# Kernel tuning notes

Hardware: AMD Instinct MI355X
Metric: run time of the kernel (lower is better)

Reference implementation:

```python
import jax, jax.numpy as jnp
import numpy as np

BN_EPS = 1e-5


def conv3x3(x, w):
    # 3x3 'same' conv, stride 1, no bias (matches nn.Conv2d(k=3, padding=1, bias=False))
    return jax.lax.conv_general_dilated(
        x, w, window_strides=(1, 1), padding='SAME',
        dimension_numbers=('NCHW', 'OIHW', 'NCHW'))


def batchnorm(x, gamma, beta, mean, var):
    # eval-mode BatchNorm2d with running stats
    scale = (gamma / jnp.sqrt(var + BN_EPS))[None, :, None, None]
    return (x - mean[None, :, None, None]) * scale + beta[None, :, None, None]


def setup_inputs() -> dict:
    key = jax.random.key(0)
    ks = jax.random.split(key, 13)
    B, C, H, W = 16, 64, 160, 160
    wshape = (C, C, 3, 3)
    inp = {
        'x': jax.random.normal(ks[0], (B, C, H, W), jnp.float32),
        'w_cv1': jax.random.normal(ks[1], wshape, jnp.float32) * 0.05,
        'g1': jax.random.uniform(ks[2], (C,), jnp.float32, 0.5, 1.5),
        'b1': jax.random.normal(ks[3], (C,), jnp.float32) * 0.1,
        'm1': jax.random.normal(ks[4], (C,), jnp.float32) * 0.1,
        'v1': jax.random.uniform(ks[5], (C,), jnp.float32, 0.5, 1.5),
        'wq': jax.random.normal(ks[6], wshape, jnp.float32) * 0.05,
        'wk': jax.random.normal(ks[7], wshape, jnp.float32) * 0.05,
        'wv': jax.random.normal(ks[8], wshape, jnp.float32) * 0.05,
        'g2': jax.random.uniform(ks[9], (C,), jnp.float32, 0.5, 1.5),
        'b2': jax.random.normal(ks[10], (C,), jnp.float32) * 0.1,
        'm2': jax.random.normal(ks[11], (C,), jnp.float32) * 0.1,
        'v2': jax.random.uniform(ks[12], (C,), jnp.float32, 0.5, 1.5),
    }
    return inp


def reference(x, w_cv1, g1, b1, m1, v1, wq, wk, wv, g2, b2, m2, v2):
    # cv1: Conv -> BN -> SiLU
    y = jax.nn.silu(batchnorm(conv3x3(x, w_cv1), g1, b1, m1, v1))

    # CSA_ConvBlock on y (c_ channels)
    fq = conv3x3(y, wq)   # [B,C,H,W]
    fk = conv3x3(y, wk)
    fv = conv3x3(y, wv)
    H, W = y.shape[2], y.shape[3]

    # Original: f_sim[b,i,j,h1,h2] = sum_w fq[b,i,h1,w]*fk[b,j,h2,w] / sqrt(W);
    # then sum over j, then mean-ish sum over (h1,h2)/H^2 -> f_scores[b,i].
    # Algebraically identical reorder (sum-before-matmul):
    k_sum = fk.sum(axis=(1, 2))                       # [B,W], sum over channels j and rows h2
    scale = 1.0 / (float(W) ** 0.5 * float(H) * float(H))
    f_scores = jnp.einsum('bchw,bw->bc', fq, k_sum) * scale  # [B,C]
    scores = jax.nn.softmax(f_scores, axis=1)[:, :, None, None]

    r = scores * fv + y
    r = jax.nn.relu(batchnorm(r, g2, b2, m2, v2))

    # shortcut: c1 == c2 and shortcut=True
    return x + r
```

## Files before the change

kernel.cpp:

```cpp
#include <hip/hip_runtime.h>
#include <hip/hip_bf16.h>
#include <math.h>

#define NB 16
#define NC 64
#define NH 160
#define NW 160

typedef __attribute__((ext_vector_type(8))) short bf16x8;
typedef __attribute__((ext_vector_type(4))) float f32x4;
typedef __attribute__((ext_vector_type(8))) unsigned short u16x8;
typedef __attribute__((ext_vector_type(4))) unsigned short u16x4;

__device__ __forceinline__ unsigned short f2bf(float v) {
  union { __hip_bfloat16 b; unsigned short u; } cv; cv.b = __float2bfloat16(v); return cv.u;
}
__device__ __forceinline__ float bf2f(unsigned short u) {
  union { unsigned u; float f; } cv; cv.u = ((unsigned)u) << 16; return cv.f;
}

#define LGKM_BARRIER()                                  \
  asm volatile("s_waitcnt lgkmcnt(0)" ::: "memory");    \
  __builtin_amdgcn_sched_barrier(0);                    \
  __builtin_amdgcn_s_barrier();                         \
  __builtin_amdgcn_sched_barrier(0);

__global__ void pack_w_kernel3(const float* __restrict__ wA, const float* __restrict__ wB,
                               const float* __restrict__ wq, const float* __restrict__ wk,
                               unsigned short* __restrict__ apkA, unsigned short* __restrict__ apkB,
                               float* __restrict__ wqt, float* __restrict__ wkst) {
  int idx = blockIdx.x * 256 + threadIdx.x;
  if (idx < 2 * 36864) {
    const float* w = (idx < 36864) ? wA : wB;
    unsigned short* apk = (idx < 36864) ? apkA : apkB;
    int i = (idx < 36864) ? idx : idx - 36864;
    int j = i & 7, l = (i >> 3) & 63, rest = i >> 9;
    int ks = rest % 18, ct = rest / 18;
    int cih = ks & 1, tap = ks >> 1, kh = tap / 3, kw = tap % 3;
    int co = ct * 16 + (l & 15), ci = cih * 32 + (l >> 4) * 8 + j;
    apk[i] = f2bf(w[(((size_t)co * NC + ci) * 3 + kh) * 3 + kw]);
  } else if (idx < 3 * 36864) {
    int i2 = idx - 2 * 36864;
    int c = i2 & 63, tau = i2 >> 6;
    int i = tau & 63, jj = tau >> 6;
    wqt[i2] = wq[(size_t)c * 576 + i * 9 + jj];
  } else if (idx < 3 * 36864 + 576) {
    int i3 = idx - 3 * 36864;
    int i = i3 & 63, jj = i3 >> 6;
    float s = 0.f;
    for (int cj = 0; cj < NC; ++cj) s += wk[(size_t)cj * 576 + i * 9 + jj];
    wkst[i3] = s;
  }
}

template<bool FINAL>
__global__ __launch_bounds__(256, 2) void conv3x3_mfma7(
    const unsigned short* __restrict__ in_nhwc, const float* __restrict__ in_nchw,
    const unsigned short* __restrict__ apk,
    const float* __restrict__ gg, const float* __restrict__ bbeta,
    const float* __restrict__ mmean, const float* __restrict__ vvar,
    void* __restrict__ outv, const float* __restrict__ scores,
    const float* __restrict__ xres, float* __restrict__ colpart)
{
  __shared__ unsigned short ring[6 * 34 * 64];
  __shared__ unsigned short epi[FINAL ? 8 : 2 * 64 * 72];
  __shared__ f32x4 csv[FINAL ? 1 : 512];

  const int t = threadIdx.x, lane = t & 63, wave = t >> 6;
  const int q = lane >> 4, col = lane & 15;

  int g = blockIdx.x;
  int sw = (g & 7) * 160 + (g >> 3);
  const int b = sw / 80;
  int rem = sw % 80;
  const int h0 = (rem / 5) * 10, w0 = (rem % 5) * 32;

  float scR[4], shR[4], scoR[4];
#pragma unroll
  for (int r = 0; r < 4; ++r) {
    int co = wave * 16 + q * 4 + r;
    float s = gg[co] * rsqrtf(vvar[co] + 1e-5f);
    scR[r] = s; shR[r] = bbeta[co] - mmean[co] * s;
    scoR[r] = FINAL ? scores[b * NC + co] : 0.f;
  }

  bf16x8 wf[18];
#pragma unroll
  for (int ks = 0; ks < 18; ++ks)
    wf[ks] = *(const bf16x8*)&apk[((size_t)(wave * 18 + ks) * 64 + lane) * 8];

  const unsigned short* inb = FINAL ? in_nhwc + (size_t)b * NH * NW * 64 : nullptr;
  const float* xb = FINAL ? nullptr : in_nchw + (size_t)b * NC * NH * NW;

#define SLOT(R) ((int)((unsigned)((R) + 1) % 6u) * 2176)

#define STGF_ISSUE(ROW, V0, V1, A0, A1)                                       \
  { int row_ = (ROW);                                                         \
    bool rowok_ = (unsigned)row_ < (unsigned)NH;                              \
    int slot_ = SLOT(row_);                                                   \
    { int wcc = t >> 3, s8 = t & 7; int wsrc = w0 + wcc - 1;                  \
      A0 = slot_ + wcc * 64 + ((s8 ^ (wcc & 7)) << 3);                        \
      V0 = (u16x8){};                                                         \
      if (rowok_ && (unsigned)wsrc < (unsigned)NW)                            \
        V0 = *(const u16x8*)&inb[((size_t)row_ * NW + wsrc) * 64 + s8 * 8];   \
    }                                                                         \
    if (t < 16) { int c = 256 + t; int wcc = c >> 3, s8 = c & 7;              \
      int wsrc = w0 + wcc - 1;                                                \
      A1 = slot_ + wcc * 64 + ((s8 ^ (wcc & 7)) << 3);                        \
      V1 = (u16x8){};                                                         \
      if (rowok_ && (unsigned)wsrc < (unsigned)NW)                            \
        V1 = *(const u16x8*)&inb[((size_t)row_ * NW + wsrc) * 64 + s8 * 8];   \
    } }
#define STGF_COMMIT(V0, V1, A0, A1)                                           \
  *(u16x8*)&ring[A0] = V0;                                                    \
  if (t < 16) *(u16x8*)&ring[A1] = V1;

#define STG1_ISSUE(ROW, F0, F1, A0, A1)                                       \
  { int row_ = (ROW);                                                         \
    bool rowok_ = (unsigned)row_ < (unsigned)NH;                              \
    int slot_ = SLOT(row_);                                                   \
    { int wcc = t % 34, s8 = t / 34; int wsrc = w0 + wcc - 1;                 \
      A0 = slot_ + wcc * 64 + ((s8 ^ (wcc & 7)) << 3);                        \
      bool ok_ = rowok_ && (unsigned)wsrc < (unsigned)NW;                     \
      if (ok_) {                                                              \
        const float* xp_ = xb + ((size_t)(s8 * 8) * NH + row_) * NW + wsrc;   \
        _Pragma("unroll") for (int j_ = 0; j_ < 8; ++j_)                      \
          F0[j_] = xp_[(size_t)j_ * NH * NW];                                 \
      } else {                                                                \
        _Pragma("unroll") for (int j_ = 0; j_ < 8; ++j_) F0[j_] = 0.f;        \
      }                                                                       \
    }                                                                         \
    if (t < 16) { int wcc = 18 + t; int wsrc = w0 + wcc - 1;                  \
      A1 = slot_ + wcc * 64 + ((7 ^ (wcc & 7)) << 3);                         \
      bool ok_ = rowok_ && (unsigned)wsrc < (unsigned)NW;                     \
      if (ok_) {                                                              \
        const float* xp_ = xb + ((size_t)56 * NH + row_) * NW + wsrc;         \
        _Pragma("unroll") for (int j_ = 0; j_ < 8; ++j_)                      \
          F1[j_] = xp_[(size_t)j_ * NH * NW];                                 \
      } else {                                                                \
        _Pragma("unroll") for (int j_ = 0; j_ < 8; ++j_) F1[j_] = 0.f;        \
      }                                                                       \
    } }
#define STG1_COMMIT(F0, F1, A0, A1)                                           \
  { u16x8 pv_;                                                                \
    _Pragma("unroll") for (int j_ = 0; j_ < 8; ++j_) pv_[j_] = f2bf(F0[j_]);  \
    *(u16x8*)&ring[A0] = pv_; }                                               \
  if (t < 16) { u16x8 pv_;                                                    \
    _Pragma("unroll") for (int j_ = 0; j_ < 8; ++j_) pv_[j_] = f2bf(F1[j_]);  \
    *(u16x8*)&ring[A1] = pv_; }

  if constexpr (!FINAL) {
    csv[t] = (f32x4){0.f, 0.f, 0.f, 0.f};
    csv[t + 256] = (f32x4){0.f, 0.f, 0.f, 0.f};
  }

  if constexpr (FINAL) {
    for (int rr = -1; rr <= 2; ++rr) {
      u16x8 v0, v1 = {}; int a0, a1 = 0;
      STGF_ISSUE(h0 + rr, v0, v1, a0, a1)
      STGF_COMMIT(v0, v1, a0, a1)
    }
  } else {
    for (int rr = -1; rr <= 2; ++rr) {
      float f0[8], f1[8]; int a0, a1 = 0;
      STG1_ISSUE(h0 + rr, f0, f1, a0, a1)
      STG1_COMMIT(f0, f1, a0, a1)
    }
  }
  LGKM_BARRIER()

  for (int wi = 0; wi < 5; ++wi) {
    const int h = h0 + wi * 2;
    const bool doS = (wi < 4);

    u16x8 va0, va1 = {}, vb0, vb1 = {}; int aa0, aa1 = 0, ab0, ab1 = 0;
    float fa0[8], fa1[8], fb0[8], fb1[8];
    if (doS) {
      if constexpr (FINAL) {
        STGF_ISSUE(h + 3, va0, va1, aa0, aa1)
        STGF_ISSUE(h + 4, vb0, vb1, ab0, ab1)
      } else {
        STG1_ISSUE(h + 3, fa0, fa1, aa0, aa1)
        STG1_ISSUE(h + 4, fb0, fb1, ab0, ab1)
      }
    }

    const int sl[4] = { SLOT(h - 1), SLOT(h), SLOT(h + 1), SLOT(h + 2) };
    f32x4 acc[2][2];
#pragma unroll
    for (int o = 0; o < 2; ++o) { acc[o][0] = (f32x4){0,0,0,0}; acc[o][1] = (f32x4){0,0,0,0}; }

#pragma unroll
    for (int ri = 0; ri < 4; ++ri) {
#pragma unroll
      for (int kw = 0; kw < 3; ++kw) {
#pragma unroll
        for (int cih = 0; cih < 2; ++cih) {
          const int wcb = col + kw;
          const int ea = sl[ri] + wcb * 64 + (((cih << 2) + q) ^ (wcb & 7)) * 8;
          const bf16x8* bp = (const bf16x8*)&ring[ea];
          bf16x8 B0 = bp[0], B1 = bp[128];
          if (ri <= 2) {
            const int ks = (ri * 3 + kw) * 2 + cih;
            acc[0][0] = __builtin_amdgcn_mfma_f32_16x16x32_bf16(wf[ks], B0, acc[0][0], 0, 0, 0);
            acc[0][1] = __builtin_amdgcn_mfma_f32_16x16x32_bf16(wf[ks], B1, acc[0][1], 0, 0, 0);
          }
          if (ri >= 1) {
            const int ks = ((ri - 1) * 3 + kw) * 2 + cih;
            acc[1][0] = __builtin_amdgcn_mfma_f32_16x16x32_bf16(wf[ks], B0, acc[1][0], 0, 0, 0);
            acc[1][1] = __builtin_amdgcn_mfma_f32_16x16x32_bf16(wf[ks], B1, acc[1][1], 0, 0, 0);
          }
        }
      }
    }

    if constexpr (!FINAL) {
      const int buf = (wi & 1) * 4608;
      f32x4 csadd[2];
      csadd[0] = (f32x4){0,0,0,0}; csadd[1] = (f32x4){0,0,0,0};
#pragma unroll
      for (int o = 0; o < 2; ++o) {
#pragma unroll
        for (int wt = 0; wt < 2; ++wt) {
          u16x4 ev;
#pragma unroll
          for (int r = 0; r < 4; ++r) {
            float z = scR[r] * acc[o][wt][r] + shR[r];
            ev[r] = f2bf(z / (1.f + __expf(-z)));
          }
          *(u16x4*)&epi[buf + ((o * 32) + wt * 16 + col) * 72 + wave * 16 + q * 4] = ev;
#pragma unroll
          for (int r = 0; r < 4; ++r) csadd[wt][r] += bf2f(ev[r]);
        }
      }
      { int cc = wave * 4 + q;
        csv[cc * 32 + col]      += csadd[0];
        csv[cc * 32 + 16 + col] += csadd[1]; }
      if (doS) { STG1_COMMIT(fa0, fa1, aa0, aa1) STG1_COMMIT(fb0, fb1, ab0, ab1) }
      LGKM_BARRIER()
      { int w = t >> 3, s = t & 7;
#pragma unroll
        for (int o = 0; o < 2; ++o) {
          unsigned short* yo = (unsigned short*)outv + (((size_t)b * NH + h + o) * NW + w0) * 64;
          *(u16x8*)&yo[w * 64 + s * 8] = *(const u16x8*)&epi[buf + ((o * 32) + w) * 72 + s * 8];
        }
      }
    } else {
      if (doS) { STGF_COMMIT(va0, va1, aa0, aa1) STGF_COMMIT(vb0, vb1, ab0, ab1) }
      float* outp = (float*)outv;
#pragma unroll
      for (int o = 0; o < 2; ++o) {
        const int rb1 = sl[1 + o];
#pragma unroll
        for (int wt = 0; wt < 2; ++wt) {
          int wcc = wt * 16 + col + 1;
          int gr = (wave * 2 + (q >> 1)) ^ (wcc & 7);
          u16x4 yv = *(const u16x4*)&ring[rb1 + wcc * 64 + gr * 8 + (q & 1) * 4];
#pragma unroll
          for (int r = 0; r < 4; ++r) {
            int co = wave * 16 + q * 4 + r;
            float rv = scoR[r] * acc[o][wt][r] + bf2f(yv[r]);
            float rb_ = scR[r] * rv + shR[r];
            rb_ = fmaxf(rb_, 0.f);
            size_t oi = (((size_t)b * NC + co) * NH + h + o) * NW + w0 + wt * 16 + col;
            outp[oi] = xres[oi] + rb_;
          }
        }
      }
      LGKM_BARRIER()
    }
  }

  if constexpr (!FINAL) {
    const int strip = h0 / 10;
    float* pp = colpart + (((size_t)b * 16 + strip) * NW + w0) * 64;
    int w = t >> 3, g0 = t & 7;
    *(f32x4*)&pp[w * 64 + g0 * 4]       = csv[g0 * 32 + w];
    *(f32x4*)&pp[w * 64 + (g0 + 8) * 4] = csv[(g0 + 8) * 32 + w];
  }
#undef STG1_ISSUE
#undef STG1_COMMIT
#undef STGF_ISSUE
#undef STGF_COMMIT
#undef SLOT
}

__global__ void colsum2_kernel(const float* __restrict__ part, float* __restrict__ ycol) {
  int id = blockIdx.x * 256 + threadIdx.x;
  if (id >= NB * NW * NC) return;
  int c = id & 63; int bw = id >> 6; int w = bw % NW; int b = bw / NW;
  const float* p = part + (((size_t)b * 16) * NW + w) * 64 + c;
  float s = 0.f;
#pragma unroll
  for (int st = 0; st < 16; ++st) s += p[(size_t)st * NW * 64];
  ycol[id] = s;
}

__device__ __forceinline__ float zval(const float* __restrict__ ycol,
                                      const unsigned short* __restrict__ y,
                                      int b, int i, int kh, int wp) {
  float z = ycol[((size_t)b * NW + wp) * 64 + i];
  if (kh == 0) z -= bf2f(y[(((size_t)b * NH + (NH - 1)) * NW + wp) * 64 + i]);
  if (kh == 2) z -= bf2f(y[(((size_t)b * NH) * NW + wp) * 64 + i]);
  return z;
}

__global__ __launch_bounds__(256) void ks_kernel(
    const float* __restrict__ ycol, const unsigned short* __restrict__ y,
    const float* __restrict__ wkst, float* __restrict__ ks)
{
  int id = blockIdx.x * 4 + (threadIdx.x >> 6);
  int lane = threadIdx.x & 63;
  int b = id / NW, w = id % NW;
  float s = 0.f;
#pragma unroll
  for (int jj = 0; jj < 9; ++jj) {
    int kh = jj / 3, kw = jj % 3;
    int wp = w + kw - 1;
    if ((unsigned)wp < (unsigned)NW)
      s += wkst[jj * 64 + lane] * zval(ycol, y, b, lane, kh, wp);
  }
#pragma unroll
  for (int off = 32; off; off >>= 1) s += __shfl_xor(s, off);
  if (lane == 0) ks[id] = s;
}

__global__ __launch_bounds__(256) void u_kernel(
    const float* __restrict__ ycol, const unsigned short* __restrict__ y,
    const float* __restrict__ ks, float* __restrict__ U)
{
  __shared__ float red[4][64];
  int bid = blockIdx.x;
  int b = bid / 9, jj = bid % 9;
  int kh = jj / 3, kw = jj % 3;
  int i = threadIdx.x & 63, ch = threadIdx.x >> 6;
  float s = 0.f;
  for (int w = ch * 40; w < ch * 40 + 40; ++w) {
    int wp = w + kw - 1;
    if ((unsigned)wp < (unsigned)NW)
      s += zval(ycol, y, b, i, kh, wp) * ks[b * NW + w];
  }
  red[ch][i] = s;
  __syncthreads();
  if (threadIdx.x < 64)
    U[((size_t)b * 9 + jj) * 64 + threadIdx.x] =
        red[0][threadIdx.x] + red[1][threadIdx.x] + red[2][threadIdx.x] + red[3][threadIdx.x];
}

__global__ __launch_bounds__(256) void scores_kernel2(
    const float* __restrict__ wqt, const float* __restrict__ U,
    float* __restrict__ scores)
{
  __shared__ float red[4][64];
  int b = blockIdx.x;
  int c = threadIdx.x & 63, p = threadIdx.x >> 6;
  const float* Ub = U + (size_t)b * 576;
  float s = 0.f;
  for (int tau = p * 144; tau < p * 144 + 144; ++tau)
    s += wqt[(size_t)tau * 64 + c] * Ub[tau];
  red[p][c] = s;
  __syncthreads();
  if (threadIdx.x < 64) {
    const float scale = 1.0f / (sqrtf((float)NW) * (float)NH * (float)NH);
    float f = (red[0][c] + red[1][c] + red[2][c] + red[3][c]) * scale;
    float mx = f;
#pragma unroll
    for (int off = 32; off; off >>= 1) mx = fmaxf(mx, __shfl_xor(mx, off));
    float e = __expf(f - mx);
    float sm = e;
#pragma unroll
    for (int off = 32; off; off >>= 1) sm += __shfl_xor(sm, off);
    scores[b * NC + c] = e / sm;
  }
}

extern "C" void kernel_launch(void* const* d_in, const int* in_sizes, int n_in,
                              void* d_out, int out_size, void* d_ws, size_t ws_size,
                              hipStream_t stream) {
  const float* x  = (const float*)d_in[0];
  const float* w1 = (const float*)d_in[1];
  const float* g1 = (const float*)d_in[2];
  const float* b1 = (const float*)d_in[3];
  const float* m1 = (const float*)d_in[4];
  const float* v1 = (const float*)d_in[5];
  const float* wq = (const float*)d_in[6];
  const float* wk = (const float*)d_in[7];
  const float* wv = (const float*)d_in[8];
  const float* g2 = (const float*)d_in[9];
  const float* b2 = (const float*)d_in[10];
  const float* m2 = (const float*)d_in[11];
  const float* v2 = (const float*)d_in[12];
  float* out = (float*)d_out;

  unsigned short* apk1 = (unsigned short*)d_ws;
  unsigned short* apk2 = apk1 + 36864;
  float* wqt  = (float*)(apk2 + 36864);
  float* wkst = wqt + 36864;
  float* ycol = wkst + 576;
  float* ks   = ycol + NB * NW * NC;
  float* U    = ks + NB * NW;
  float* scr  = U + NB * 576;
  float* part = scr + 1024;
  unsigned short* y = (unsigned short*)(part + (size_t)NB * 16 * NW * 64);

  pack_w_kernel3<<<dim3(435), 256, 0, stream>>>(w1, wv, wq, wk, apk1, apk2, wqt, wkst);

  conv3x3_mfma7<false><<<dim3(1280), 256, 0, stream>>>(
      nullptr, x, apk1, g1, b1, m1, v1, (void*)y, nullptr, nullptr, part);

  colsum2_kernel<<<dim3((NB * NW * NC + 255) / 256), 256, 0, stream>>>(part, ycol);
  ks_kernel<<<dim3(NB * NW / 4), 256, 0, stream>>>(ycol, y, wkst, ks);
  u_kernel<<<dim3(NB * 9), 256, 0, stream>>>(ycol, y, ks, U);
  scores_kernel2<<<dim3(NB), 256, 0, stream>>>(wqt, U, scr);

  conv3x3_mfma7<true><<<dim3(1280), 256, 0, stream>>>(
      y, nullptr, apk2, g2, b2, m2, v2, (void*)out, scr, x, nullptr);
}
```

Baseline: 150.4 us.

## Deepen row prefetch pipeline, preload residual, and raise MFMA wave priority

Row staging changes from a one-step in-iteration load to a two-row-ahead software pipeline. Global loads for rows h+5/h+6 are issued before the MFMA loop and committed to the LDS ring at the start of the next iteration, and the prologue overlaps pairs of row loads. The final pass also loads the residual x values before the MFMA loop instead of in the epilogue, and s_setprio raises wave priority around the MFMA block. The aim is to hide global memory latency behind compute, at the cost of more live registers, which could cause spills at 2 blocks per CU. Correctness depends on the ring slots not being overwritten while still being read.

```diff
diff --git a/kernel.cpp b/kernel.cpp
--- a/kernel.cpp
+++ b/kernel.cpp
@@ -54,7 +54,7 @@
 }
 
 template<bool FINAL>
-__global__ __launch_bounds__(256, 2) void conv3x3_mfma7(
+__global__ __launch_bounds__(256, 2) void conv3x3_mfma8(
     const unsigned short* __restrict__ in_nhwc, const float* __restrict__ in_nchw,
     const unsigned short* __restrict__ apk,
     const float* __restrict__ gg, const float* __restrict__ bbeta,
@@ -154,35 +154,67 @@
     csv[t + 256] = (f32x4){0.f, 0.f, 0.f, 0.f};
   }
 
+  u16x8 pva0, pva1 = {}, pvb0, pvb1 = {};
+  float pfa0[8], pfa1[8], pfb0[8], pfb1[8];
+  int paa0, paa1 = 0, pab0, pab1 = 0;
+
   if constexpr (FINAL) {
-    for (int rr = -1; rr <= 2; ++rr) {
-      u16x8 v0, v1 = {}; int a0, a1 = 0;
-      STGF_ISSUE(h0 + rr, v0, v1, a0, a1)
-      STGF_COMMIT(v0, v1, a0, a1)
-    }
+    { u16x8 v0, v1 = {}, w0v, w1v = {}; int a0, a1 = 0, b0a, b1a = 0;
+      STGF_ISSUE(h0 - 1, v0, v1, a0, a1)
+      STGF_ISSUE(h0,     w0v, w1v, b0a, b1a)
+      STGF_COMMIT(v0, v1, a0, a1) STGF_COMMIT(w0v, w1v, b0a, b1a)
+      STGF_ISSUE(h0 + 1, v0, v1, a0, a1)
+      STGF_ISSUE(h0 + 2, w0v, w1v, b0a, b1a)
+      STGF_COMMIT(v0, v1, a0, a1) STGF_COMMIT(w0v, w1v, b0a, b1a) }
+    STGF_ISSUE(h0 + 3, pva0, pva1, paa0, paa1)
+    STGF_ISSUE(h0 + 4, pvb0, pvb1, pab0, pab1)
   } else {
-    for (int rr = -1; rr <= 2; ++rr) {
-      float f0[8], f1[8]; int a0, a1 = 0;
-      STG1_ISSUE(h0 + rr, f0, f1, a0, a1)
-      STG1_COMMIT(f0, f1, a0, a1)
-    }
+    { float f0[8], f1[8], g0[8], g1[8]; int a0, a1 = 0, b0a, b1a = 0;
+      STG1_ISSUE(h0 - 1, f0, f1, a0, a1)
+      STG1_ISSUE(h0,     g0, g1, b0a, b1a)
+      STG1_COMMIT(f0, f1, a0, a1) STG1_COMMIT(g0, g1, b0a, b1a)
+      STG1_ISSUE(h0 + 1, f0, f1, a0, a1)
+      STG1_ISSUE(h0 + 2, g0, g1, b0a, b1a)
+      STG1_COMMIT(f0, f1, a0, a1) STG1_COMMIT(g0, g1, b0a, b1a) }
+    STG1_ISSUE(h0 + 3, pfa0, pfa1, paa0, paa1)
+    STG1_ISSUE(h0 + 4, pfb0, pfb1, pab0, pab1)
   }
   LGKM_BARRIER()
 
+#pragma unroll
   for (int wi = 0; wi < 5; ++wi) {
     const int h = h0 + wi * 2;
-    const bool doS = (wi < 4);
-
-    u16x8 va0, va1 = {}, vb0, vb1 = {}; int aa0, aa1 = 0, ab0, ab1 = 0;
-    float fa0[8], fa1[8], fb0[8], fb1[8];
-    if (doS) {
+
+    if (wi < 4) {
       if constexpr (FINAL) {
-        STGF_ISSUE(h + 3, va0, va1, aa0, aa1)
-        STGF_ISSUE(h + 4, vb0, vb1, ab0, ab1)
+        STGF_COMMIT(pva0, pva1, paa0, paa1)
+        STGF_COMMIT(pvb0, pvb1, pab0, pab1)
       } else {
-        STG1_ISSUE(h + 3, fa0, fa1, aa0, aa1)
-        STG1_ISSUE(h + 4, fb0, fb1, ab0, ab1)
-      }
+        STG1_COMMIT(pfa0, pfa1, paa0, paa1)
+        STG1_COMMIT(pfb0, pfb1, pab0, pab1)
+      }
+    }
+    if (wi < 3) {
+      if constexpr (FINAL) {
+        STGF_ISSUE(h + 5, pva0, pva1, paa0, paa1)
+        STGF_ISSUE(h + 6, pvb0, pvb1, pab0, pab1)
+      } else {
+        STG1_ISSUE(h + 5, pfa0, pfa1, paa0, paa1)
+        STG1_ISSUE(h + 6, pfb0, pfb1, pab0, pab1)
+      }
+    }
+
+    float xrv[2][2][4];
+    if constexpr (FINAL) {
+#pragma unroll
+      for (int o = 0; o < 2; ++o)
+#pragma unroll
+        for (int wt = 0; wt < 2; ++wt)
+#pragma unroll
+          for (int r = 0; r < 4; ++r) {
+            int co = wave * 16 + q * 4 + r;
+            xrv[o][wt][r] = xres[(((size_t)b * NC + co) * NH + h + o) * NW + w0 + wt * 16 + col];
+          }
     }
 
     const int sl[4] = { SLOT(h - 1), SLOT(h), SLOT(h + 1), SLOT(h + 2) };
@@ -190,6 +222,7 @@
 #pragma unroll
     for (int o = 0; o < 2; ++o) { acc[o][0] = (f32x4){0,0,0,0}; acc[o][1] = (f32x4){0,0,0,0}; }
 
+    __builtin_amdgcn_s_setprio(1);
 #pragma unroll
     for (int ri = 0; ri < 4; ++ri) {
 #pragma unroll
@@ -213,6 +246,7 @@
         }
       }
     }
+    __builtin_amdgcn_s_setprio(0);
 
     if constexpr (!FINAL) {
       const int buf = (wi & 1) * 4608;
@@ -236,7 +270,6 @@
       { int cc = wave * 4 + q;
         csv[cc * 32 + col]      += csadd[0];
         csv[cc * 32 + 16 + col] += csadd[1]; }
-      if (doS) { STG1_COMMIT(fa0, fa1, aa0, aa1) STG1_COMMIT(fb0, fb1, ab0, ab1) }
       LGKM_BARRIER()
       { int w = t >> 3, s = t & 7;
 #pragma unroll
@@ -246,7 +279,6 @@
         }
       }
     } else {
-      if (doS) { STGF_COMMIT(va0, va1, aa0, aa1) STGF_COMMIT(vb0, vb1, ab0, ab1) }
       float* outp = (float*)outv;
 #pragma unroll
       for (int o = 0; o < 2; ++o) {
@@ -263,7 +295,7 @@
             float rb_ = scR[r] * rv + shR[r];
             rb_ = fmaxf(rb_, 0.f);
             size_t oi = (((size_t)b * NC + co) * NH + h + o) * NW + w0 + wt * 16 + col;
-            outp[oi] = xres[oi] + rb_;
+            outp[oi] = xrv[o][wt][r] + rb_;
           }
         }
       }
@@ -405,7 +437,7 @@
 
   pack_w_kernel3<<<dim3(435), 256, 0, stream>>>(w1, wv, wq, wk, apk1, apk2, wqt, wkst);
 
-  conv3x3_mfma7<false><<<dim3(1280), 256, 0, stream>>>(
+  conv3x3_mfma8<false><<<dim3(1280), 256, 0, stream>>>(
       nullptr, x, apk1, g1, b1, m1, v1, (void*)y, nullptr, nullptr, part);
 
   colsum2_kernel<<<dim3((NB * NW * NC + 255) / 256), 256, 0, stream>>>(part, ycol);
@@ -413,6 +445,6 @@
   u_kernel<<<dim3(NB * 9), 256, 0, stream>>>(ycol, y, ks, U);
   scores_kernel2<<<dim3(NB), 256, 0, stream>>>(wqt, U, scr);
 
-  conv3x3_mfma7<true><<<dim3(1280), 256, 0, stream>>>(
+  conv3x3_mfma8<true><<<dim3(1280), 256, 0, stream>>>(
       y, nullptr, apk2, g2, b2, m2, v2, (void*)out, scr, x, nullptr);
 }
```

Measured after the change: 162.5 us. 8.1% more time.

## Compute three output rows per window with deeper ring and register column sums

Applied to the files above, without the earlier changes.

The conv kernel now splits each 10-row strip into 3+3+2+2 output rows instead of five 2-row windows, with a fully unrolled schedule and an 8-slot input ring. Each staged input row then feeds more MFMAs per barrier, and there are fewer barriers and window iterations. Column sums stay in registers and are written once through the reused epilogue buffer, which removes the per-window LDS read-modify-write. In exchange the kernel holds more accumulators and needs more LDS, which may cut occupancy at the launch bound of 2 blocks per CU.

```diff
diff --git a/kernel.cpp b/kernel.cpp
--- a/kernel.cpp
+++ b/kernel.cpp
@@ -54,7 +54,7 @@
 }
 
 template<bool FINAL>
-__global__ __launch_bounds__(256, 2) void conv3x3_mfma7(
+__global__ __launch_bounds__(256, 2) void conv3x3_mfma10(
     const unsigned short* __restrict__ in_nhwc, const float* __restrict__ in_nchw,
     const unsigned short* __restrict__ apk,
     const float* __restrict__ gg, const float* __restrict__ bbeta,
@@ -62,9 +62,8 @@
     void* __restrict__ outv, const float* __restrict__ scores,
     const float* __restrict__ xres, float* __restrict__ colpart)
 {
-  __shared__ unsigned short ring[6 * 34 * 64];
-  __shared__ unsigned short epi[FINAL ? 8 : 2 * 64 * 72];
-  __shared__ f32x4 csv[FINAL ? 1 : 512];
+  __shared__ unsigned short ring[8 * 34 * 64];
+  __shared__ unsigned short epi[FINAL ? 8 : 2 * 3 * 32 * 72];
 
   const int t = threadIdx.x, lane = t & 63, wave = t >> 6;
   const int q = lane >> 4, col = lane & 15;
@@ -89,10 +88,14 @@
   for (int ks = 0; ks < 18; ++ks)
     wf[ks] = *(const bf16x8*)&apk[((size_t)(wave * 18 + ks) * 64 + lane) * 8];
 
+  f32x4 csreg[2];
+  csreg[0] = (f32x4){0.f, 0.f, 0.f, 0.f};
+  csreg[1] = (f32x4){0.f, 0.f, 0.f, 0.f};
+
   const unsigned short* inb = FINAL ? in_nhwc + (size_t)b * NH * NW * 64 : nullptr;
   const float* xb = FINAL ? nullptr : in_nchw + (size_t)b * NC * NH * NW;
 
-#define SLOT(R) ((int)((unsigned)((R) + 1) % 6u) * 2176)
+#define SLOT(R) ((int)((unsigned)((R) + 1) % 8u) * 2176)
 
 #define STGF_ISSUE(ROW, V0, V1, A0, A1)                                       \
   { int row_ = (ROW);                                                         \
@@ -149,139 +152,171 @@
     _Pragma("unroll") for (int j_ = 0; j_ < 8; ++j_) pv_[j_] = f2bf(F1[j_]);  \
     *(u16x8*)&ring[A1] = pv_; }
 
+#define COMPUTE_RI(NR, RI)                                                    \
+  { const int slr = SLOT(h - 1 + (RI));                                       \
+    _Pragma("unroll") for (int kw = 0; kw < 3; ++kw) {                        \
+      _Pragma("unroll") for (int cih = 0; cih < 2; ++cih) {                   \
+        const int wcb = col + kw;                                             \
+        const int ea = slr + wcb * 64 + (((cih << 2) + q) ^ (wcb & 7)) * 8;   \
+        const bf16x8* bp = (const bf16x8*)&ring[ea];                          \
+        bf16x8 B0 = bp[0], B1 = bp[128];                                      \
+        _Pragma("unroll") for (int o = 0; o < (NR); ++o) {                    \
+          if (o <= (RI) && (RI) - o <= 2) {                                   \
+            const int ksx = (((RI) - o) * 3 + kw) * 2 + cih;                  \
+            acc[o][0] = __builtin_amdgcn_mfma_f32_16x16x32_bf16(wf[ksx], B0, acc[o][0], 0, 0, 0); \
+            acc[o][1] = __builtin_amdgcn_mfma_f32_16x16x32_bf16(wf[ksx], B1, acc[o][1], 0, 0, 0); \
+          } } } } }
+
+#define EPILOGUE(NR, WI)                                                      \
+    if constexpr (!FINAL) {                                                   \
+      const int buf = ((WI) & 1) * 6912;                                      \
+      _Pragma("unroll") for (int o = 0; o < (NR); ++o) {                      \
+        _Pragma("unroll") for (int wt = 0; wt < 2; ++wt) {                    \
+          u16x4 ev;                                                           \
+          _Pragma("unroll") for (int r = 0; r < 4; ++r) {                     \
+            float z = scR[r] * acc[o][wt][r] + shR[r];                        \
+            ev[r] = f2bf(z / (1.f + __expf(-z)));                             \
+          }                                                                   \
+          *(u16x4*)&epi[buf + ((o * 32) + wt * 16 + col) * 72 + wave * 16 + q * 4] = ev; \
+          _Pragma("unroll") for (int r = 0; r < 4; ++r)                       \
+            csreg[wt][r] += bf2f(ev[r]);                                      \
+        } }                                                                   \
+      LGKM_BARRIER()                                                          \
+      { int w_ = t >> 3, s_ = t & 7;                                          \
+        _Pragma("unroll") for (int o = 0; o < (NR); ++o) {                    \
+          unsigned short* yo = (unsigned short*)outv +                        \
+              (((size_t)b * NH + h + o) * NW + w0) * 64;                      \
+          *(u16x8*)&yo[w_ * 64 + s_ * 8] =                                    \
+              *(const u16x8*)&epi[buf + ((o * 32) + w_) * 72 + s_ * 8];       \
+        } }                                                                   \
+    } else {                                                                  \
+      float* outp = (float*)outv;                                             \
+      _Pragma("unroll") for (int o = 0; o < (NR); ++o) {                      \
+        const int rb1 = SLOT(h + o);                                          \
+        _Pragma("unroll") for (int wt = 0; wt < 2; ++wt) {                    \
+          int wcc = wt * 16 + col + 1;                                        \
+          int gr = (wave * 2 + (q >> 1)) ^ (wcc & 7);                         \
+          u16x4 yv = *(const u16x4*)&ring[rb1 + wcc * 64 + gr * 8 + (q & 1) * 4]; \
+          _Pragma("unroll") for (int r = 0; r < 4; ++r) {                     \
+            int co = wave * 16 + q * 4 + r;                                   \
+            float rv = scoR[r] * acc[o][wt][r] + bf2f(yv[r]);                 \
+            float rb_ = scR[r] * rv + shR[r];                                 \
+            rb_ = fmaxf(rb_, 0.f);                                            \
+            size_t oi = (((size_t)b * NC + co) * NH + h + o) * NW + w0 + wt * 16 + col; \
+            outp[oi] = xres[oi] + rb_;                                        \
+          } } }                                                               \
+      LGKM_BARRIER()                                                          \
+    }
+
+#define DO_WIN3(WI, HOFF, SN)                                                 \
+  { const int h = h0 + (HOFF);                                                \
+    u16x8 v10, v11 = {}, v20, v21 = {};                                       \
+    float f10[8], f11[8], f20[8], f21[8];                                     \
+    int a10 = 0, a11 = 0, a20 = 0, a21 = 0;                                   \
+    if constexpr (FINAL) {                                                    \
+      if ((SN) >= 1) STGF_ISSUE(h + 4, v10, v11, a10, a11)                    \
+      if ((SN) >= 2) STGF_ISSUE(h + 5, v20, v21, a20, a21)                    \
+    } else {                                                                  \
+      if ((SN) >= 1) STG1_ISSUE(h + 4, f10, f11, a10, a11)                    \
+      if ((SN) >= 2) STG1_ISSUE(h + 5, f20, f21, a20, a21)                    \
+    }                                                                         \
+    f32x4 acc[3][2];                                                          \
+    _Pragma("unroll") for (int o = 0; o < 3; ++o) {                           \
+      acc[o][0] = (f32x4){0.f,0.f,0.f,0.f}; acc[o][1] = (f32x4){0.f,0.f,0.f,0.f}; } \
+    COMPUTE_RI(3, 0) COMPUTE_RI(3, 1)                                         \
+    if constexpr (FINAL) {                                                    \
+      if ((SN) >= 1) { STGF_COMMIT(v10, v11, a10, a11) }                      \
+      if ((SN) >= 2) { STGF_COMMIT(v20, v21, a20, a21) }                      \
+      if ((SN) >= 3) STGF_ISSUE(h + 6, v10, v11, a10, a11)                    \
+    } else {                                                                  \
+      if ((SN) >= 1) { STG1_COMMIT(f10, f11, a10, a11) }                      \
+      if ((SN) >= 2) { STG1_COMMIT(f20, f21, a20, a21) }                      \
+      if ((SN) >= 3) STG1_ISSUE(h + 6, f10, f11, a10, a11)                    \
+    }                                                                         \
+    COMPUTE_RI(3, 2) COMPUTE_RI(3, 3) COMPUTE_RI(3, 4)                        \
+    if constexpr (FINAL) {                                                    \
+      if ((SN) >= 3) { STGF_COMMIT(v10, v11, a10, a11) }                      \
+    } else {                                                                  \
+      if ((SN) >= 3) { STG1_COMMIT(f10, f11, a10, a11) }                      \
+    }                                                                         \
+    EPILOGUE(3, WI)                                                           \
+  }
+
+#define DO_WIN2(WI, HOFF, SN)                                                 \
+  { const int h = h0 + (HOFF);                                                \
+    u16x8 v10, v11 = {}, v20, v21 = {};                                       \
+    float f10[8], f11[8], f20[8], f21[8];                                     \
+    int a10 = 0, a11 = 0, a20 = 0, a21 = 0;                                   \
+    if constexpr (FINAL) {                                                    \
+      if ((SN) >= 1) STGF_ISSUE(h + 3, v10, v11, a10, a11)                    \
+      if ((SN) >= 2) STGF_ISSUE(h + 4, v20, v21, a20, a21)                    \
+    } else {                                                                  \
+      if ((SN) >= 1) STG1_ISSUE(h + 3, f10, f11, a10, a11)                    \
+      if ((SN) >= 2) STG1_ISSUE(h + 4, f20, f21, a20, a21)                    \
+    }                                                                         \
+    f32x4 acc[2][2];                                                          \
+    _Pragma("unroll") for (int o = 0; o < 2; ++o) {                           \
+      acc[o][0] = (f32x4){0.f,0.f,0.f,0.f}; acc[o][1] = (f32x4){0.f,0.f,0.f,0.f}; } \
+    COMPUTE_RI(2, 0) COMPUTE_RI(2, 1)                                         \
+    if constexpr (FINAL) {                                                    \
+      if ((SN) >= 1) { STGF_COMMIT(v10, v11, a10, a11) }                      \
+      if ((SN) >= 2) { STGF_COMMIT(v20, v21, a20, a21) }                      \
+    } else {                                                                  \
+      if ((SN) >= 1) { STG1_COMMIT(f10, f11, a10, a11) }                      \
+      if ((SN) >= 2) { STG1_COMMIT(f20, f21, a20, a21) }                      \
+    }                                                                         \
+    COMPUTE_RI(2, 2) COMPUTE_RI(2, 3)                                         \
+    EPILOGUE(2, WI)                                                           \
+  }
+
+  if constexpr (FINAL) {
+    u16x8 v10, v11 = {}, v20, v21 = {}; int a10 = 0, a11 = 0, a20 = 0, a21 = 0;
+    STGF_ISSUE(h0 - 1, v10, v11, a10, a11)
+    STGF_ISSUE(h0,     v20, v21, a20, a21)
+    STGF_COMMIT(v10, v11, a10, a11) STGF_COMMIT(v20, v21, a20, a21)
+    STGF_ISSUE(h0 + 1, v10, v11, a10, a11)
+    STGF_ISSUE(h0 + 2, v20, v21, a20, a21)
+    STGF_COMMIT(v10, v11, a10, a11) STGF_COMMIT(v20, v21, a20, a21)
+    STGF_ISSUE(h0 + 3, v10, v11, a10, a11)
+    STGF_COMMIT(v10, v11, a10, a11)
+  } else {
+    float f10[8], f11[8], f20[8], f21[8]; int a10 = 0, a11 = 0, a20 = 0, a21 = 0;
+    STG1_ISSUE(h0 - 1, f10, f11, a10, a11)
+    STG1_ISSUE(h0,     f20, f21, a20, a21)
+    STG1_COMMIT(f10, f11, a10, a11) STG1_COMMIT(f20, f21, a20, a21)
+    STG1_ISSUE(h0 + 1, f10, f11, a10, a11)
+    STG1_ISSUE(h0 + 2, f20, f21, a20, a21)
+    STG1_COMMIT(f10, f11, a10, a11) STG1_COMMIT(f20, f21, a20, a21)
+    STG1_ISSUE(h0 + 3, f10, f11, a10, a11)
+    STG1_COMMIT(f10, f11, a10, a11)
+  }
+  LGKM_BARRIER()
+
+  DO_WIN3(0, 0, 3)
+  DO_WIN3(1, 3, 2)
+  DO_WIN2(2, 6, 2)
+  DO_WIN2(3, 8, 0)
+
   if constexpr (!FINAL) {
-    csv[t] = (f32x4){0.f, 0.f, 0.f, 0.f};
-    csv[t + 256] = (f32x4){0.f, 0.f, 0.f, 0.f};
-  }
-
-  if constexpr (FINAL) {
-    for (int rr = -1; rr <= 2; ++rr) {
-      u16x8 v0, v1 = {}; int a0, a1 = 0;
-      STGF_ISSUE(h0 + rr, v0, v1, a0, a1)
-      STGF_COMMIT(v0, v1, a0, a1)
-    }
-  } else {
-    for (int rr = -1; rr <= 2; ++rr) {
-      float f0[8], f1[8]; int a0, a1 = 0;
-      STG1_ISSUE(h0 + rr, f0, f1, a0, a1)
-      STG1_COMMIT(f0, f1, a0, a1)
-    }
-  }
-  LGKM_BARRIER()
-
-  for (int wi = 0; wi < 5; ++wi) {
-    const int h = h0 + wi * 2;
-    const bool doS = (wi < 4);
-
-    u16x8 va0, va1 = {}, vb0, vb1 = {}; int aa0, aa1 = 0, ab0, ab1 = 0;
-    float fa0[8], fa1[8], fb0[8], fb1[8];
-    if (doS) {
-      if constexpr (FINAL) {
-        STGF_ISSUE(h + 3, va0, va1, aa0, aa1)
-        STGF_ISSUE(h + 4, vb0, vb1, ab0, ab1)
-      } else {
-        STG1_ISSUE(h + 3, fa0, fa1, aa0, aa1)
-        STG1_ISSUE(h + 4, fb0, fb1, ab0, ab1)
-      }
-    }
-
-    const int sl[4] = { SLOT(h - 1), SLOT(h), SLOT(h + 1), SLOT(h + 2) };
-    f32x4 acc[2][2];
-#pragma unroll
-    for (int o = 0; o < 2; ++o) { acc[o][0] = (f32x4){0,0,0,0}; acc[o][1] = (f32x4){0,0,0,0}; }
-
-#pragma unroll
-    for (int ri = 0; ri < 4; ++ri) {
-#pragma unroll
-      for (int kw = 0; kw < 3; ++kw) {
-#pragma unroll
-        for (int cih = 0; cih < 2; ++cih) {
-          const int wcb = col + kw;
-          const int ea = sl[ri] + wcb * 64 + (((cih << 2) + q) ^ (wcb & 7)) * 8;
-          const bf16x8* bp = (const bf16x8*)&ring[ea];
-          bf16x8 B0 = bp[0], B1 = bp[128];
-          if (ri <= 2) {
-            const int ks = (ri * 3 + kw) * 2 + cih;
-            acc[0][0] = __builtin_amdgcn_mfma_f32_16x16x32_bf16(wf[ks], B0, acc[0][0], 0, 0, 0);
-            acc[0][1] = __builtin_amdgcn_mfma_f32_16x16x32_bf16(wf[ks], B1, acc[0][1], 0, 0, 0);
-          }
-          if (ri >= 1) {
-            const int ks = ((ri - 1) * 3 + kw) * 2 + cih;
-            acc[1][0] = __builtin_amdgcn_mfma_f32_16x16x32_bf16(wf[ks], B0, acc[1][0], 0, 0, 0);
-            acc[1][1] = __builtin_amdgcn_mfma_f32_16x16x32_bf16(wf[ks], B1, acc[1][1], 0, 0, 0);
-          }
-        }
-      }
-    }
-
-    if constexpr (!FINAL) {
-      const int buf = (wi & 1) * 4608;
-      f32x4 csadd[2];
-      csadd[0] = (f32x4){0,0,0,0}; csadd[1] = (f32x4){0,0,0,0};
-#pragma unroll
-      for (int o = 0; o < 2; ++o) {
-#pragma unroll
-        for (int wt = 0; wt < 2; ++wt) {
-          u16x4 ev;
-#pragma unroll
-          for (int r = 0; r < 4; ++r) {
-            float z = scR[r] * acc[o][wt][r] + shR[r];
-            ev[r] = f2bf(z / (1.f + __expf(-z)));
-          }
-          *(u16x4*)&epi[buf + ((o * 32) + wt * 16 + col) * 72 + wave * 16 + q * 4] = ev;
-#pragma unroll
-          for (int r = 0; r < 4; ++r) csadd[wt][r] += bf2f(ev[r]);
-        }
-      }
-      { int cc = wave * 4 + q;
-        csv[cc * 32 + col]      += csadd[0];
-        csv[cc * 32 + 16 + col] += csadd[1]; }
-      if (doS) { STG1_COMMIT(fa0, fa1, aa0, aa1) STG1_COMMIT(fb0, fb1, ab0, ab1) }
-      LGKM_BARRIER()
-      { int w = t >> 3, s = t & 7;
-#pragma unroll
-        for (int o = 0; o < 2; ++o) {
-          unsigned short* yo = (unsigned short*)outv + (((size_t)b * NH + h + o) * NW + w0) * 64;
-          *(u16x8*)&yo[w * 64 + s * 8] = *(const u16x8*)&epi[buf + ((o * 32) + w) * 72 + s * 8];
-        }
-      }
-    } else {
-      if (doS) { STGF_COMMIT(va0, va1, aa0, aa1) STGF_COMMIT(vb0, vb1, ab0, ab1) }
-      float* outp = (float*)outv;
-#pragma unroll
-      for (int o = 0; o < 2; ++o) {
-        const int rb1 = sl[1 + o];
-#pragma unroll
-        for (int wt = 0; wt < 2; ++wt) {
-          int wcc = wt * 16 + col + 1;
-          int gr = (wave * 2 + (q >> 1)) ^ (wcc & 7);
-          u16x4 yv = *(const u16x4*)&ring[rb1 + wcc * 64 + gr * 8 + (q & 1) * 4];
-#pragma unroll
-          for (int r = 0; r < 4; ++r) {
-            int co = wave * 16 + q * 4 + r;
-            float rv = scoR[r] * acc[o][wt][r] + bf2f(yv[r]);
-            float rb_ = scR[r] * rv + shR[r];
-            rb_ = fmaxf(rb_, 0.f);
-            size_t oi = (((size_t)b * NC + co) * NH + h + o) * NW + w0 + wt * 16 + col;
-            outp[oi] = xres[oi] + rb_;
-          }
-        }
-      }
-      LGKM_BARRIER()
-    }
-  }
-
-  if constexpr (!FINAL) {
+    f32x4* csvL = (f32x4*)epi;
+    { int cc = wave * 4 + q;
+      csvL[cc * 32 + col]      = csreg[0];
+      csvL[cc * 32 + 16 + col] = csreg[1]; }
+    LGKM_BARRIER()
     const int strip = h0 / 10;
     float* pp = colpart + (((size_t)b * 16 + strip) * NW + w0) * 64;
     int w = t >> 3, g0 = t & 7;
-    *(f32x4*)&pp[w * 64 + g0 * 4]       = csv[g0 * 32 + w];
-    *(f32x4*)&pp[w * 64 + (g0 + 8) * 4] = csv[(g0 + 8) * 32 + w];
+    *(f32x4*)&pp[w * 64 + g0 * 4]       = csvL[g0 * 32 + w];
+    *(f32x4*)&pp[w * 64 + (g0 + 8) * 4] = csvL[(g0 + 8) * 32 + w];
   }
 #undef STG1_ISSUE
 #undef STG1_COMMIT
 #undef STGF_ISSUE
 #undef STGF_COMMIT
+#undef COMPUTE_RI
+#undef EPILOGUE
+#undef DO_WIN3
+#undef DO_WIN2
 #undef SLOT
 }
 
@@ -405,7 +440,7 @@
 
   pack_w_kernel3<<<dim3(435), 256, 0, stream>>>(w1, wv, wq, wk, apk1, apk2, wqt, wkst);
 
-  conv3x3_mfma7<false><<<dim3(1280), 256, 0, stream>>>(
+  conv3x3_mfma10<false><<<dim3(1280), 256, 0, stream>>>(
       nullptr, x, apk1, g1, b1, m1, v1, (void*)y, nullptr, nullptr, part);
 
   colsum2_kernel<<<dim3((NB * NW * NC + 255) / 256), 256, 0, stream>>>(part, ycol);
@@ -413,6 +448,6 @@
   u_kernel<<<dim3(NB * 9), 256, 0, stream>>>(ycol, y, ks, U);
   scores_kernel2<<<dim3(NB), 256, 0, stream>>>(wqt, U, scr);
 
-  conv3x3_mfma7<true><<<dim3(1280), 256, 0, stream>>>(
+  conv3x3_mfma10<true><<<dim3(1280), 256, 0, stream>>>(
       y, nullptr, apk2, g2, b2, m2, v2, (void*)out, scr, x, nullptr);
 }
```

After: 174.8 us. 16.2% more time.
